# Optimization experiments

Measured on AMD Instinct MI355X. Metric: run time of the kernel, lower is better.

The kernel has to match this reference:

```python
import jax, jax.numpy as jnp
import numpy as np

K_LAYERS = 10
ALPHA = 0.1
N_NODES = 100000
N_EDGES = 500000
N_PATHS = 3
D = 128
HID = 128


def setup_inputs() -> dict:
    key = jax.random.key(0)
    k1, k2, k3, k4 = jax.random.split(key, 4)
    h = jax.random.normal(k1, (N_NODES, D), dtype=jnp.float32)
    edges = jax.random.randint(k2, (N_PATHS, 2, N_EDGES), 0, N_NODES, dtype=jnp.int64)
    W1 = jax.random.normal(k3, (D, HID), dtype=jnp.float32) * (1.0 / np.sqrt(D))
    b1 = jnp.zeros((HID,), dtype=jnp.float32)
    w2 = jax.random.normal(k4, (HID, 1), dtype=jnp.float32) * (1.0 / np.sqrt(HID))
    return {"h": h, "edges": edges, "W1": W1, "b1": b1, "w2": w2}


def _appnp(h0, src, dst):
    # DGL APPNPConv (eval mode, no dropout): symmetric degree normalization,
    # K steps of h <- (1-alpha) * D_in^{-1/2} A D_out^{-1/2} h + alpha * h0
    n = h0.shape[0]
    ones = jnp.ones(src.shape[0], dtype=h0.dtype)
    out_deg = jnp.clip(jax.ops.segment_sum(ones, src, num_segments=n), 1.0)
    in_deg = jnp.clip(jax.ops.segment_sum(ones, dst, num_segments=n), 1.0)
    norm_s = out_deg ** -0.5  # [N]
    norm_d = in_deg ** -0.5   # [N]

    def step(x, _):
        msg = (x * norm_s[:, None])[src]                       # [E, D] gather
        agg = jax.ops.segment_sum(msg, dst, num_segments=n)    # [N, D] scatter-add
        x = (1.0 - ALPHA) * (agg * norm_d[:, None]) + ALPHA * h0
        return x, None

    x, _ = jax.lax.scan(step, h0, None, length=K_LAYERS)
    return x


def reference(h, edges, W1, b1, w2):
    src = edges[:, 0, :]  # [P, E]
    dst = edges[:, 1, :]
    # one APPNP propagation per meta-path, vmapped over the P axis
    z = jax.vmap(lambda s, d: _appnp(h, s, d))(src, dst)  # [P, N, D]
    z = jnp.transpose(z, (1, 0, 2))                        # [N, P, D]
    # semantic attention: small MLP -> mean over nodes -> softmax over paths
    w = jnp.tanh(z @ W1 + b1) @ w2   # [N, P, 1]
    w = w.mean(axis=0)               # [P, 1]
    beta = jax.nn.softmax(w, axis=0) # [P, 1]
    return (beta[None, :, :] * z).sum(axis=1)  # [N, D]
```

## Files before the change

### kernel.cpp

```cpp
#include <hip/hip_runtime.h>
#include <math.h>

#define N_NODES 100000
#define N_EDGES 500000
#define N_PATHS 3
#define DIM 128
#define K_LAYERS 10
#define NBLK_PER_PATH ((N_NODES + 255) / 256)
#define PN (N_PATHS * N_NODES)
#define HRANGE 8192
#define NRANGE ((N_NODES + HRANGE - 1) / HRANGE)
#define BPG 16

typedef __attribute__((ext_vector_type(8))) short bf16x8;
typedef __attribute__((ext_vector_type(4))) float f32x4;

__device__ __forceinline__ float bflo(unsigned u) { return __uint_as_float(u << 16); }
__device__ __forceinline__ float bfhi(unsigned u) { return __uint_as_float(u & 0xffff0000u); }

__global__ __launch_bounds__(256) void hist_kernel(const int* __restrict__ edges,
                                                   int* __restrict__ partial) {
    __shared__ int hist[HRANGE];
    int g = blockIdx.x / BPG;
    int b = blockIdx.x - g * BPG;
    int r = g % NRANGE;
    int pt = g / NRANGE;
    int p = pt >> 1, t = pt & 1;
    for (int i = threadIdx.x; i < HRANGE; i += 256) hist[i] = 0;
    __syncthreads();

    const int4* arr4 = (const int4*)(edges + ((size_t)p * 2 + t) * N_EDGES);
    const int n4 = N_EDGES / 4;
    const int stride = BPG * 256;
    int lo = r * HRANGE;

    int i4 = b * 256 + threadIdx.x;
    int4 cur = make_int4(-1, -1, -1, -1);
    if (i4 < n4) cur = arr4[i4];
    while (i4 < n4) {
        int ni = i4 + stride;
        int4 nxt = make_int4(-1, -1, -1, -1);
        if (ni < n4) nxt = arr4[ni];
        int v0 = cur.x - lo, v1 = cur.y - lo, v2 = cur.z - lo, v3 = cur.w - lo;
        if ((unsigned)v0 < HRANGE) atomicAdd(&hist[v0], 1);
        if ((unsigned)v1 < HRANGE) atomicAdd(&hist[v1], 1);
        if ((unsigned)v2 < HRANGE) atomicAdd(&hist[v2], 1);
        if ((unsigned)v3 < HRANGE) atomicAdd(&hist[v3], 1);
        cur = nxt;
        i4 = ni;
    }
    __syncthreads();
    int* outp = partial + ((size_t)g * BPG + b) * HRANGE;
    for (int i = threadIdx.x; i < HRANGE; i += 256) outp[i] = hist[i];
}

__global__ __launch_bounds__(256) void deg_reduce_kernel(const int* __restrict__ partial,
                                                         float* __restrict__ norm_s,
                                                         float* __restrict__ norm_d,
                                                         int* __restrict__ degD_tot) {
    int i = blockIdx.x * 256 + threadIdx.x;
    if (i >= PN) return;
    int p = i / N_NODES, n = i - p * N_NODES;
    int r = n / HRANGE, off = n - r * HRANGE;
    const int* ps = partial + (((size_t)(p * 2 + 0) * NRANGE + r) * BPG) * HRANGE + off;
    const int* pd = partial + (((size_t)(p * 2 + 1) * NRANGE + r) * BPG) * HRANGE + off;
    int sS = 0, sD = 0;
#pragma unroll
    for (int b = 0; b < BPG; ++b) {
        sS += ps[(size_t)b * HRANGE];
        sD += pd[(size_t)b * HRANGE];
    }
    norm_s[i] = 1.0f / sqrtf(fmaxf((float)sS, 1.0f));
    norm_d[i] = 1.0f / sqrtf(fmaxf((float)sD, 1.0f));
    degD_tot[i] = sD;
}

__global__ __launch_bounds__(256) void blocksum_kernel(const int* __restrict__ cnt,
                                                       int* __restrict__ bsum) {
    int b = blockIdx.x;
    int p = b / NBLK_PER_PATH;
    int lb = b - p * NBLK_PER_PATH;
    int idx = lb * 256 + threadIdx.x;
    int v = (idx < N_NODES) ? cnt[p * N_NODES + idx] : 0;
#pragma unroll
    for (int off = 32; off; off >>= 1) v += __shfl_xor(v, off);
    __shared__ int ws[4];
    if ((threadIdx.x & 63) == 0) ws[threadIdx.x >> 6] = v;
    __syncthreads();
    if (threadIdx.x == 0) bsum[b] = ws[0] + ws[1] + ws[2] + ws[3];
}

__global__ __launch_bounds__(512) void bscan_kernel(int* __restrict__ bsum) {
    __shared__ int s[512];
    int p = blockIdx.x;
    int t = threadIdx.x;
    int v = (t < NBLK_PER_PATH) ? bsum[p * NBLK_PER_PATH + t] : 0;
    s[t] = v;
    __syncthreads();
    for (int off = 1; off < 512; off <<= 1) {
        int x = s[t];
        int a = (t >= off) ? s[t - off] : 0;
        __syncthreads();
        s[t] = x + a;
        __syncthreads();
    }
    if (t < NBLK_PER_PATH) bsum[p * NBLK_PER_PATH + t] = s[t] - v;
}

__global__ __launch_bounds__(256) void scan_write_kernel(const int* __restrict__ cnt,
                                                         const int* __restrict__ bsum,
                                                         int* __restrict__ row_ptr_all,
                                                         int* __restrict__ cursor_all) {
    __shared__ int s[256];
    int b = blockIdx.x;
    int p = b / NBLK_PER_PATH;
    int lb = b - p * NBLK_PER_PATH;
    int idx = lb * 256 + threadIdx.x;
    int t = threadIdx.x;
    int v = (idx < N_NODES) ? cnt[p * N_NODES + idx] : 0;
    s[t] = v;
    __syncthreads();
    for (int off = 1; off < 256; off <<= 1) {
        int x = s[t];
        int a = (t >= off) ? s[t - off] : 0;
        __syncthreads();
        s[t] = x + a;
        __syncthreads();
    }
    int excl = s[t] - v + bsum[b];
    if (idx < N_NODES) {
        row_ptr_all[p * (N_NODES + 1) + idx] = excl;
        cursor_all[p * N_NODES + idx] = excl;
        if (idx == N_NODES - 1)
            row_ptr_all[p * (N_NODES + 1) + N_NODES] = excl + v;
    }
}

__global__ __launch_bounds__(256) void fill_kernel(const int* __restrict__ edges,
                                                   const float* __restrict__ norm_s,
                                                   const float* __restrict__ norm_d,
                                                   int* __restrict__ cursor,
                                                   int2* __restrict__ cw) {
    int idx = blockIdx.x * 256 + threadIdx.x;
    if (idx < N_PATHS * N_EDGES) {
        int p = idx / N_EDGES;
        int e = idx - p * N_EDGES;
        const int* src = edges + (size_t)p * 2 * N_EDGES;
        const int* dst = src + N_EDGES;
        int s = src[e], d = dst[e];
        int pos = atomicAdd(&cursor[p * N_NODES + d], 1);
        float w = 0.9f * norm_s[p * N_NODES + s] * norm_d[p * N_NODES + d];
        cw[(size_t)p * N_EDGES + pos] = make_int2(s, __float_as_int(w));
    }
}

__device__ __forceinline__ unsigned bf16pack(float a, float b) {
    unsigned ua = __float_as_uint(a), ub = __float_as_uint(b);
    ua = (ua + 0x7fffu + ((ua >> 16) & 1)) >> 16;
    ub = (ub + 0x7fffu + ((ub >> 16) & 1)) >> 16;
    return ua | (ub << 16);
}

__global__ __launch_bounds__(256) void cast_kernel(const float4* __restrict__ in,
                                                   ushort4* __restrict__ outp) {
    int idx = blockIdx.x * 256 + threadIdx.x;
    if (idx < N_NODES * DIM / 4) {
        float4 v = in[idx];
        ushort4 o;
        unsigned u;
        u = __float_as_uint(v.x); o.x = (unsigned short)((u + 0x7fff + ((u >> 16) & 1)) >> 16);
        u = __float_as_uint(v.y); o.y = (unsigned short)((u + 0x7fff + ((u >> 16) & 1)) >> 16);
        u = __float_as_uint(v.z); o.z = (unsigned short)((u + 0x7fff + ((u >> 16) & 1)) >> 16);
        u = __float_as_uint(v.w); o.w = (unsigned short)((u + 0x7fff + ((u >> 16) & 1)) >> 16);
        outp[idx] = o;
    }
}

__global__ __launch_bounds__(256) void w1t_kernel(const float* __restrict__ W1,
                                                  unsigned short* __restrict__ W1t) {
    int idx = blockIdx.x * 256 + threadIdx.x;
    if (idx < DIM * DIM) {
        int c = idx >> 7, k = idx & 127;
        unsigned u = __float_as_uint(W1[k * DIM + c]);
        W1t[idx] = (unsigned short)((u + 0x7fff + ((u >> 16) & 1)) >> 16);
    }
}

template <int OUT_F32, int H_BF16>
__global__ __launch_bounds__(256) void prop_kernel(const unsigned short* __restrict__ xin,
                                                   size_t in_stride,
                                                   const void* __restrict__ anchor,
                                                   void* __restrict__ xout,
                                                   const int* __restrict__ row_ptr,
                                                   const int2* __restrict__ cw) {
    int wid  = threadIdx.x >> 6;
    int lane = threadIdx.x & 63;
    int oct  = lane >> 3;
    int ol   = lane & 7;
    int nodeBase = blockIdx.x * 32 + wid * 8;
    int p  = nodeBase / N_NODES;
    int nb = nodeBase - p * N_NODES;
    const int*  rp   = row_ptr + p * (N_NODES + 1);
    const int2* cwp  = cw + (size_t)p * N_EDGES;
    const uint4* xin4 = (const uint4*)(xin + (size_t)p * in_stride);

    int rv = 0;
    if (lane < 9) rv = rp[nb + lane];
    int beg = __shfl(rv, oct);
    int end = __shfl(rv, oct + 1);
    int deg = end - beg;
    int myNode = nb + oct;
    int maxd = deg;
    maxd = max(maxd, __shfl_xor(maxd, 8));
    maxd = max(maxd, __shfl_xor(maxd, 16));
    maxd = max(maxd, __shfl_xor(maxd, 32));

    float a0 = 0.f, a1 = 0.f, a2 = 0.f, a3 = 0.f;
    float a4 = 0.f, a5 = 0.f, a6 = 0.f, a7 = 0.f;
    float a8 = 0.f, a9 = 0.f, a10 = 0.f, a11 = 0.f;
    float a12 = 0.f, a13 = 0.f, a14 = 0.f, a15 = 0.f;

    for (int base = 0; base < maxd; base += 8) {
        int2 e = make_int2(0, 0);
        if (base + ol < deg) e = cwp[beg + base + ol];
        int lim = maxd - base; if (lim > 8) lim = 8;
#pragma unroll 4
        for (int j = 0; j < lim; ++j) {
            int lsrc = (lane & 56) | j;
            int   c = __shfl(e.x, lsrc);
            float w = __int_as_float(__shfl(e.y, lsrc));
            if (base + j < deg) {
                uint4 v1 = xin4[(size_t)c * 16 + ol];
                uint4 v2 = xin4[(size_t)c * 16 + 8 + ol];
                a0  = fmaf(w, bflo(v1.x), a0);  a1  = fmaf(w, bfhi(v1.x), a1);
                a2  = fmaf(w, bflo(v1.y), a2);  a3  = fmaf(w, bfhi(v1.y), a3);
                a4  = fmaf(w, bflo(v1.z), a4);  a5  = fmaf(w, bfhi(v1.z), a5);
                a6  = fmaf(w, bflo(v1.w), a6);  a7  = fmaf(w, bfhi(v1.w), a7);
                a8  = fmaf(w, bflo(v2.x), a8);  a9  = fmaf(w, bfhi(v2.x), a9);
                a10 = fmaf(w, bflo(v2.y), a10); a11 = fmaf(w, bfhi(v2.y), a11);
                a12 = fmaf(w, bflo(v2.z), a12); a13 = fmaf(w, bfhi(v2.z), a13);
                a14 = fmaf(w, bflo(v2.w), a14); a15 = fmaf(w, bfhi(v2.w), a15);
            }
        }
    }

    if (H_BF16) {
        uint4 hv1 = ((const uint4*)anchor)[(size_t)myNode * 16 + ol];
        uint4 hv2 = ((const uint4*)anchor)[(size_t)myNode * 16 + 8 + ol];
        a0  += 0.1f * bflo(hv1.x); a1  += 0.1f * bfhi(hv1.x);
        a2  += 0.1f * bflo(hv1.y); a3  += 0.1f * bfhi(hv1.y);
        a4  += 0.1f * bflo(hv1.z); a5  += 0.1f * bfhi(hv1.z);
        a6  += 0.1f * bflo(hv1.w); a7  += 0.1f * bfhi(hv1.w);
        a8  += 0.1f * bflo(hv2.x); a9  += 0.1f * bfhi(hv2.x);
        a10 += 0.1f * bflo(hv2.y); a11 += 0.1f * bfhi(hv2.y);
        a12 += 0.1f * bflo(hv2.z); a13 += 0.1f * bfhi(hv2.z);
        a14 += 0.1f * bflo(hv2.w); a15 += 0.1f * bfhi(hv2.w);
    } else {
        const float4* h4 = (const float4*)anchor + (size_t)myNode * 32;
        float4 p0 = h4[ol * 2], p1 = h4[ol * 2 + 1];
        float4 p2 = h4[ol * 2 + 16], p3 = h4[ol * 2 + 17];
        a0  += 0.1f * p0.x; a1  += 0.1f * p0.y; a2  += 0.1f * p0.z; a3  += 0.1f * p0.w;
        a4  += 0.1f * p1.x; a5  += 0.1f * p1.y; a6  += 0.1f * p1.z; a7  += 0.1f * p1.w;
        a8  += 0.1f * p2.x; a9  += 0.1f * p2.y; a10 += 0.1f * p2.z; a11 += 0.1f * p2.w;
        a12 += 0.1f * p3.x; a13 += 0.1f * p3.y; a14 += 0.1f * p3.z; a15 += 0.1f * p3.w;
    }

    size_t row = (size_t)p * N_NODES + myNode;
    if (OUT_F32) {
        float4* zo = (float4*)xout + row * 32;
        zo[ol * 2]      = make_float4(a0, a1, a2, a3);
        zo[ol * 2 + 1]  = make_float4(a4, a5, a6, a7);
        zo[ol * 2 + 16] = make_float4(a8, a9, a10, a11);
        zo[ol * 2 + 17] = make_float4(a12, a13, a14, a15);
    } else {
        uint4 o1, o2;
        o1.x = bf16pack(a0, a1);   o1.y = bf16pack(a2, a3);
        o1.z = bf16pack(a4, a5);   o1.w = bf16pack(a6, a7);
        o2.x = bf16pack(a8, a9);   o2.y = bf16pack(a10, a11);
        o2.z = bf16pack(a12, a13); o2.w = bf16pack(a14, a15);
        ((uint4*)xout)[row * 16 + ol]     = o1;
        ((uint4*)xout)[row * 16 + 8 + ol] = o2;
    }
}

__device__ __forceinline__ float fast_tanh(float x) {
    float e = __expf(2.0f * x);
    return 1.0f - 2.0f / (e + 1.0f);
}

__global__ __launch_bounds__(256) void attn_kernel(const float* __restrict__ z,
                                                   const unsigned short* __restrict__ W1t,
                                                   const float* __restrict__ b1,
                                                   const float* __restrict__ w2,
                                                   float* __restrict__ wsum) {
    const int wid  = threadIdx.x >> 6;
    const int lane = threadIdx.x & 63;
    const int c0   = lane & 15;
    const int kh   = lane >> 4;

    const bf16x8* w1t8 = (const bf16x8*)W1t;
    bf16x8 Bf[8][4];
#pragma unroll
    for (int nt = 0; nt < 8; ++nt)
#pragma unroll
        for (int ks = 0; ks < 4; ++ks)
            Bf[nt][ks] = w1t8[(nt * 16 + c0) * 16 + ks * 4 + kh];

    float b1v[8], w2v[8];
#pragma unroll
    for (int nt = 0; nt < 8; ++nt) {
        b1v[nt] = b1[nt * 16 + c0];
        w2v[nt] = w2[nt * 16 + c0];
    }

    float accP0 = 0.f, accP1 = 0.f, accP2 = 0.f;
    const int NTILES = N_PATHS * N_NODES / 16;
    const int TPP    = N_NODES / 16;
    const int stride = gridDim.x * 4;
    const float4* zf4 = (const float4*)z;

    for (int t = blockIdx.x * 4 + wid; t < NTILES; t += stride) {
        size_t rbase = ((size_t)t * 16 + c0) * 32 + kh * 2;
        bf16x8 Af[4];
#pragma unroll
        for (int ks = 0; ks < 4; ++ks) {
            float4 x0 = zf4[rbase + ks * 8];
            float4 x1 = zf4[rbase + ks * 8 + 1];
            union { uint4 u; bf16x8 v; } cv;
            cv.u.x = bf16pack(x0.x, x0.y);
            cv.u.y = bf16pack(x0.z, x0.w);
            cv.u.z = bf16pack(x1.x, x1.y);
            cv.u.w = bf16pack(x1.z, x1.w);
            Af[ks] = cv.v;
        }
        f32x4 acc[8];
#pragma unroll
        for (int nt = 0; nt < 8; ++nt) acc[nt] = (f32x4){0.f, 0.f, 0.f, 0.f};
#pragma unroll
        for (int nt = 0; nt < 8; ++nt)
#pragma unroll
            for (int ks = 0; ks < 4; ++ks)
                acc[nt] = __builtin_amdgcn_mfma_f32_16x16x32_bf16(Af[ks], Bf[nt][ks], acc[nt], 0, 0, 0);

        float psum = 0.f;
#pragma unroll
        for (int nt = 0; nt < 8; ++nt) {
            psum += fast_tanh(acc[nt][0] + b1v[nt]) * w2v[nt];
            psum += fast_tanh(acc[nt][1] + b1v[nt]) * w2v[nt];
            psum += fast_tanh(acc[nt][2] + b1v[nt]) * w2v[nt];
            psum += fast_tanh(acc[nt][3] + b1v[nt]) * w2v[nt];
        }
#pragma unroll
        for (int off = 32; off; off >>= 1) psum += __shfl_xor(psum, off);
        if (lane == 0) {
            int p = t / TPP;
            if (p == 0) accP0 += psum;
            else if (p == 1) accP1 += psum;
            else accP2 += psum;
        }
    }
    if (lane == 0) {
        if (accP0 != 0.f) atomicAdd(&wsum[0], accP0);
        if (accP1 != 0.f) atomicAdd(&wsum[1], accP1);
        if (accP2 != 0.f) atomicAdd(&wsum[2], accP2);
    }
}

__global__ void beta_kernel(const float* __restrict__ wsum, float* __restrict__ beta) {
    if (threadIdx.x == 0 && blockIdx.x == 0) {
        float w0 = wsum[0] * (1.0f / N_NODES);
        float w1 = wsum[1] * (1.0f / N_NODES);
        float w2v = wsum[2] * (1.0f / N_NODES);
        float m = fmaxf(w0, fmaxf(w1, w2v));
        float e0 = expf(w0 - m), e1 = expf(w1 - m), e2 = expf(w2v - m);
        float inv = 1.0f / (e0 + e1 + e2);
        beta[0] = e0 * inv;
        beta[1] = e1 * inv;
        beta[2] = e2 * inv;
    }
}

__global__ __launch_bounds__(256) void combine_kernel(const float4* __restrict__ z4,
                                                      const float* __restrict__ beta,
                                                      float4* __restrict__ out4) {
    size_t idx = (size_t)blockIdx.x * 256 + threadIdx.x;
    const size_t M = (size_t)N_NODES * 32;
    if (idx < M) {
        float b0 = beta[0], b1 = beta[1], b2 = beta[2];
        float4 a = z4[idx];
        float4 b = z4[M + idx];
        float4 c = z4[2 * M + idx];
        float4 o;
        o.x = b0 * a.x + b1 * b.x + b2 * c.x;
        o.y = b0 * a.y + b1 * b.y + b2 * c.y;
        o.z = b0 * a.z + b1 * b.z + b2 * c.z;
        o.w = b0 * a.w + b1 * b.w + b2 * c.w;
        out4[idx] = o;
    }
}

extern "C" void kernel_launch(void* const* d_in, const int* in_sizes, int n_in,
                              void* d_out, int out_size, void* d_ws, size_t ws_size,
                              hipStream_t stream) {
    const float* h     = (const float*)d_in[0];
    const int*   edges = (const int*)d_in[1];
    const float* W1    = (const float*)d_in[2];
    const float* b1    = (const float*)d_in[3];
    const float* w2    = (const float*)d_in[4];
    float* out = (float*)d_out;

    char* ws = (char*)d_ws;
    float* z = (float*)ws;               ws += (size_t)N_PATHS * N_NODES * DIM * 4;
    unsigned short* buf0 = (unsigned short*)ws; ws += (size_t)N_PATHS * N_NODES * DIM * 2;
    int2* cw = (int2*)ws;                ws += (size_t)N_PATHS * N_EDGES * 8;
    int* row_ptr = (int*)ws;             ws += (size_t)N_PATHS * (N_NODES + 1) * 4 + 12;
    float* norm_s = (float*)ws;          ws += (size_t)PN * 4;
    float* norm_d = (float*)ws;          ws += (size_t)PN * 4;
    int* bsum = (int*)ws;                ws += (size_t)N_PATHS * NBLK_PER_PATH * 4;
    float* wsum = (float*)ws;            ws += 4 * 4;
    float* beta = (float*)ws;            ws += 4 * 4;
    unsigned short* W1t = (unsigned short*)ws; ws += (size_t)DIM * DIM * 2;
    int* partial  = (int*)buf0;
    int* degD_tot = partial + (size_t)3 * 2 * NRANGE * BPG * HRANGE;
    int* cursor   = degD_tot + PN;
    unsigned short* buf1 = (unsigned short*)z;
    unsigned short* hb   = (unsigned short*)z + (size_t)N_PATHS * N_NODES * DIM;

    const size_t PSTRIDE = (size_t)N_NODES * DIM;

    hist_kernel<<<3 * 2 * NRANGE * BPG, 256, 0, stream>>>(edges, partial);
    deg_reduce_kernel<<<(PN + 255) / 256, 256, 0, stream>>>(partial, norm_s, norm_d, degD_tot);
    blocksum_kernel<<<N_PATHS * NBLK_PER_PATH, 256, 0, stream>>>(degD_tot, bsum);
    bscan_kernel<<<N_PATHS, 512, 0, stream>>>(bsum);
    scan_write_kernel<<<N_PATHS * NBLK_PER_PATH, 256, 0, stream>>>(degD_tot, bsum, row_ptr, cursor);
    fill_kernel<<<(N_PATHS * N_EDGES + 255) / 256, 256, 0, stream>>>(edges, norm_s, norm_d, cursor, cw);

    cast_kernel<<<(N_NODES * DIM / 4 + 255) / 256, 256, 0, stream>>>(
        (const float4*)h, (ushort4*)hb);
    w1t_kernel<<<(DIM * DIM + 255) / 256, 256, 0, stream>>>(W1, W1t);

    const int pgrid = PN / 32;
    prop_kernel<0, 1><<<pgrid, 256, 0, stream>>>(hb, 0, hb, buf0, row_ptr, cw);
    for (int i = 1; i <= 8; ++i) {
        const unsigned short* src_b = (i & 1) ? buf0 : buf1;
        unsigned short* dst_b       = (i & 1) ? buf1 : buf0;
        prop_kernel<0, 1><<<pgrid, 256, 0, stream>>>(src_b, PSTRIDE, hb, dst_b, row_ptr, cw);
    }
    prop_kernel<1, 0><<<pgrid, 256, 0, stream>>>(buf0, PSTRIDE, h, z, row_ptr, cw);

    hipMemsetAsync(wsum, 0, 3 * 4, stream);
    attn_kernel<<<512, 256, 0, stream>>>(z, W1t, b1, w2, wsum);
    beta_kernel<<<1, 64, 0, stream>>>(wsum, beta);
    combine_kernel<<<(N_NODES * 32 + 255) / 256, 256, 0, stream>>>(
        (const float4*)z, beta, (float4*)out);
}
```

Measured before the change: 1.050 ms.

## Sort nodes by in-degree bucket so prop waves process similar-degree nodes

Adds a counting-sort pass (bucket histogram, scan, scatter) that builds a per-path permutation of nodes grouped by in-degree. The propagation kernel then processes nodes in permuted order, so the eight nodes sharing a wavefront have similar degrees and fewer lanes idle in the max-degree loop. Output rows are written through the permuted node index, which scatters writes and breaks locality of row_ptr reads. The attention kernel grid is also enlarged.

```diff
diff --git a/kernel.cpp b/kernel.cpp
--- a/kernel.cpp
+++ b/kernel.cpp
@@ -11,6 +11,7 @@
 #define HRANGE 8192
 #define NRANGE ((N_NODES + HRANGE - 1) / HRANGE)
 #define BPG 16
+#define NBUCKET 64
 
 typedef __attribute__((ext_vector_type(8))) short bf16x8;
 typedef __attribute__((ext_vector_type(4))) float f32x4;
@@ -75,6 +76,63 @@
     degD_tot[i] = sD;
 }
 
+__global__ __launch_bounds__(256) void bhist_kernel(const int* __restrict__ degD_tot,
+                                                    int* __restrict__ bcount) {
+    __shared__ int h[3 * NBUCKET];
+    for (int i = threadIdx.x; i < 3 * NBUCKET; i += 256) h[i] = 0;
+    __syncthreads();
+    int i = blockIdx.x * 256 + threadIdx.x;
+    if (i < PN) {
+        int p = i / N_NODES;
+        int b = min(degD_tot[i], NBUCKET - 1);
+        atomicAdd(&h[p * NBUCKET + b], 1);
+    }
+    __syncthreads();
+    for (int i2 = threadIdx.x; i2 < 3 * NBUCKET; i2 += 256)
+        if (h[i2]) atomicAdd(&bcount[i2], h[i2]);
+}
+
+__global__ void bscan_kernel(const int* __restrict__ bcount, int* __restrict__ bcursor) {
+    __shared__ int s[3 * NBUCKET];
+    int t = threadIdx.x;
+    int v = bcount[t];
+    s[t] = v;
+    __syncthreads();
+    for (int off = 1; off < NBUCKET; off <<= 1) {
+        int x = s[t];
+        int add = ((t & (NBUCKET - 1)) >= off) ? s[t - off] : 0;
+        __syncthreads();
+        s[t] = x + add;
+        __syncthreads();
+    }
+    bcursor[t] = s[t] - v;
+}
+
+__global__ __launch_bounds__(256) void bscatter_kernel(const int* __restrict__ degD_tot,
+                                                       int* __restrict__ bcursor,
+                                                       int* __restrict__ perm) {
+    __shared__ int h[3 * NBUCKET];
+    __shared__ int base[3 * NBUCKET];
+    for (int i = threadIdx.x; i < 3 * NBUCKET; i += 256) h[i] = 0;
+    __syncthreads();
+    int i = blockIdx.x * 256 + threadIdx.x;
+    int p = 0, n = 0, bk = 0, rank = 0;
+    bool act = i < PN;
+    if (act) {
+        p = i / N_NODES;
+        n = i - p * N_NODES;
+        bk = min(degD_tot[i], NBUCKET - 1);
+        rank = atomicAdd(&h[p * NBUCKET + bk], 1);
+    }
+    __syncthreads();
+    for (int i2 = threadIdx.x; i2 < 3 * NBUCKET; i2 += 256) {
+        int c = h[i2];
+        base[i2] = c ? atomicAdd(&bcursor[i2], c) : 0;
+    }
+    __syncthreads();
+    if (act) perm[p * N_NODES + base[p * NBUCKET + bk] + rank] = n;
+}
+
 __global__ __launch_bounds__(256) void blocksum_kernel(const int* __restrict__ cnt,
                                                        int* __restrict__ bsum) {
     int b = blockIdx.x;
@@ -90,7 +148,7 @@
     if (threadIdx.x == 0) bsum[b] = ws[0] + ws[1] + ws[2] + ws[3];
 }
 
-__global__ __launch_bounds__(512) void bscan_kernel(int* __restrict__ bsum) {
+__global__ __launch_bounds__(512) void pscan_kernel(int* __restrict__ bsum) {
     __shared__ int s[512];
     int p = blockIdx.x;
     int t = threadIdx.x;
@@ -192,7 +250,8 @@
                                                    const void* __restrict__ anchor,
                                                    void* __restrict__ xout,
                                                    const int* __restrict__ row_ptr,
-                                                   const int2* __restrict__ cw) {
+                                                   const int2* __restrict__ cw,
+                                                   const int* __restrict__ perm) {
     int wid  = threadIdx.x >> 6;
     int lane = threadIdx.x & 63;
     int oct  = lane >> 3;
@@ -202,14 +261,15 @@
     int nb = nodeBase - p * N_NODES;
     const int*  rp   = row_ptr + p * (N_NODES + 1);
     const int2* cwp  = cw + (size_t)p * N_EDGES;
+    const int*  pmp  = perm + p * N_NODES;
     const uint4* xin4 = (const uint4*)(xin + (size_t)p * in_stride);
 
-    int rv = 0;
-    if (lane < 9) rv = rp[nb + lane];
+    int pidx = (lane < 16) ? pmp[nb + (lane & 7)] : 0;
+    int rv   = (lane < 16) ? rp[pidx + (lane >> 3)] : 0;
     int beg = __shfl(rv, oct);
-    int end = __shfl(rv, oct + 1);
+    int end = __shfl(rv, oct + 8);
     int deg = end - beg;
-    int myNode = nb + oct;
+    int myNode = __shfl(pidx, oct);
     int maxd = deg;
     maxd = max(maxd, __shfl_xor(maxd, 8));
     maxd = max(maxd, __shfl_xor(maxd, 16));
@@ -420,6 +480,9 @@
     float* wsum = (float*)ws;            ws += 4 * 4;
     float* beta = (float*)ws;            ws += 4 * 4;
     unsigned short* W1t = (unsigned short*)ws; ws += (size_t)DIM * DIM * 2;
+    int* perm = (int*)ws;                ws += (size_t)PN * 4;
+    int* bcount = (int*)ws;              ws += 3 * NBUCKET * 4;
+    int* bcursor = (int*)ws;             ws += 3 * NBUCKET * 4;
     int* partial  = (int*)buf0;
     int* degD_tot = partial + (size_t)3 * 2 * NRANGE * BPG * HRANGE;
     int* cursor   = degD_tot + PN;
@@ -430,8 +493,12 @@
 
     hist_kernel<<<3 * 2 * NRANGE * BPG, 256, 0, stream>>>(edges, partial);
     deg_reduce_kernel<<<(PN + 255) / 256, 256, 0, stream>>>(partial, norm_s, norm_d, degD_tot);
+    hipMemsetAsync(bcount, 0, 3 * NBUCKET * 4, stream);
+    bhist_kernel<<<(PN + 255) / 256, 256, 0, stream>>>(degD_tot, bcount);
+    bscan_kernel<<<1, 3 * NBUCKET, 0, stream>>>(bcount, bcursor);
+    bscatter_kernel<<<(PN + 255) / 256, 256, 0, stream>>>(degD_tot, bcursor, perm);
     blocksum_kernel<<<N_PATHS * NBLK_PER_PATH, 256, 0, stream>>>(degD_tot, bsum);
-    bscan_kernel<<<N_PATHS, 512, 0, stream>>>(bsum);
+    pscan_kernel<<<N_PATHS, 512, 0, stream>>>(bsum);
     scan_write_kernel<<<N_PATHS * NBLK_PER_PATH, 256, 0, stream>>>(degD_tot, bsum, row_ptr, cursor);
     fill_kernel<<<(N_PATHS * N_EDGES + 255) / 256, 256, 0, stream>>>(edges, norm_s, norm_d, cursor, cw);
 
@@ -440,16 +507,16 @@
     w1t_kernel<<<(DIM * DIM + 255) / 256, 256, 0, stream>>>(W1, W1t);
 
     const int pgrid = PN / 32;
-    prop_kernel<0, 1><<<pgrid, 256, 0, stream>>>(hb, 0, hb, buf0, row_ptr, cw);
+    prop_kernel<0, 1><<<pgrid, 256, 0, stream>>>(hb, 0, hb, buf0, row_ptr, cw, perm);
     for (int i = 1; i <= 8; ++i) {
         const unsigned short* src_b = (i & 1) ? buf0 : buf1;
         unsigned short* dst_b       = (i & 1) ? buf1 : buf0;
-        prop_kernel<0, 1><<<pgrid, 256, 0, stream>>>(src_b, PSTRIDE, hb, dst_b, row_ptr, cw);
-    }
-    prop_kernel<1, 0><<<pgrid, 256, 0, stream>>>(buf0, PSTRIDE, h, z, row_ptr, cw);
+        prop_kernel<0, 1><<<pgrid, 256, 0, stream>>>(src_b, PSTRIDE, hb, dst_b, row_ptr, cw, perm);
+    }
+    prop_kernel<1, 0><<<pgrid, 256, 0, stream>>>(buf0, PSTRIDE, h, z, row_ptr, cw, perm);
 
     hipMemsetAsync(wsum, 0, 3 * 4, stream);
-    attn_kernel<<<512, 256, 0, stream>>>(z, W1t, b1, w2, wsum);
+    attn_kernel<<<2344, 256, 0, stream>>>(z, W1t, b1, w2, wsum);
     beta_kernel<<<1, 64, 0, stream>>>(wsum, beta);
     combine_kernel<<<(N_NODES * 32 + 255) / 256, 256, 0, stream>>>(
         (const float4*)z, beta, (float4*)out);
```

After: 1.293 ms. 1.23x slower.
